# Performance work log

Hardware: AMD Instinct MI355X
Metric: run time of the kernel (lower is better)

The kernel has to match this reference:

```python
import jax, jax.numpy as jnp
import numpy as np

B = 128
C_IN = 1
HID = 256
LAT = 256
NC = 4096
NA = 16
G = 4
DH = 256        # DynamicsModel default hidden_dim
CE = DH // 2    # code/action embed dim
IMG = 64
COMMIT = 0.25
DN = ('NCHW', 'OIHW', 'NCHW')


def conv_s2(x, w, b):
    y = jax.lax.conv_general_dilated(x, w, (2, 2), ((1, 1), (1, 1)), dimension_numbers=DN)
    return y + b[None, :, None, None]


def deconv_s2(x, w, b):
    # torch ConvTranspose2d(k=4, s=2, p=1): flip kernel, swap I/O channels,
    wt = jnp.flip(w, (2, 3)).transpose(1, 0, 2, 3)
    y = jax.lax.conv_general_dilated(x, wt, (1, 1), ((2, 2), (2, 2)),
                                     lhs_dilation=(2, 2), dimension_numbers=DN)
    return y + b[None, :, None, None]


def setup_inputs():
    key = jax.random.key(0)
    ks = iter(jax.random.split(key, 64))

    def W(shape, fan_in):
        return jax.random.normal(next(ks), shape, jnp.float32) * np.float32(1.0 / np.sqrt(fan_in))

    inp = {}
    inp['x'] = jax.random.uniform(next(ks), (B, C_IN, IMG, IMG), jnp.float32)
    inp['x_next'] = jax.random.uniform(next(ks), (B, C_IN, IMG, IMG), jnp.float32)
    inp['action'] = jax.random.randint(next(ks), (B,), 0, NA)
    # encoder Conv2d weights: [out, in, 4, 4]
    inp['enc_w1'] = W((HID, C_IN, 4, 4), C_IN * 16); inp['enc_b1'] = jnp.zeros((HID,), jnp.float32)
    inp['enc_w2'] = W((HID, HID, 4, 4), HID * 16);   inp['enc_b2'] = jnp.zeros((HID,), jnp.float32)
    inp['enc_w3'] = W((HID, HID, 4, 4), HID * 16);   inp['enc_b3'] = jnp.zeros((HID,), jnp.float32)
    inp['enc_w4'] = W((LAT, HID, 4, 4), HID * 16);   inp['enc_b4'] = jnp.zeros((LAT,), jnp.float32)
    # decoder ConvTranspose2d weights: [in, out, 4, 4]
    inp['dec_w1'] = W((LAT, HID, 4, 4), LAT * 4);    inp['dec_b1'] = jnp.zeros((HID,), jnp.float32)
    inp['dec_w2'] = W((HID, HID, 4, 4), HID * 4);    inp['dec_b2'] = jnp.zeros((HID,), jnp.float32)
    inp['dec_w3'] = W((HID, HID, 4, 4), HID * 4);    inp['dec_b3'] = jnp.zeros((HID,), jnp.float32)
    inp['dec_w4'] = W((HID, C_IN, 4, 4), HID * 4);   inp['dec_b4'] = jnp.zeros((C_IN,), jnp.float32)
    inp['codebook'] = jax.random.normal(next(ks), (NC, LAT), jnp.float32)
    inp['code_embed'] = W((NC, CE), CE)
    inp['action_embed'] = W((NA, CE), CE)
    d_in = G * G * CE + CE
    inp['dyn_w1'] = W((d_in, DH), d_in);      inp['dyn_b1'] = jnp.zeros((DH,), jnp.float32)
    inp['dyn_w2'] = W((DH, DH), DH);          inp['dyn_b2'] = jnp.zeros((DH,), jnp.float32)
    inp['dyn_w3'] = W((DH, G * G * NC), DH);  inp['dyn_b3'] = jnp.zeros((G * G * NC,), jnp.float32)
    return inp


def reference(x, x_next, action,
              enc_w1, enc_b1, enc_w2, enc_b2, enc_w3, enc_b3, enc_w4, enc_b4,
              dec_w1, dec_b1, dec_w2, dec_b2, dec_w3, dec_b3, dec_w4, dec_b4,
              codebook, code_embed, action_embed,
              dyn_w1, dyn_b1, dyn_w2, dyn_b2, dyn_w3, dyn_b3):
    relu = jax.nn.relu
    sg = jax.lax.stop_gradient

    cb_sq = jnp.sum(codebook * codebook, axis=1)  # [NC]

    def encode(xi):
        h = relu(conv_s2(xi, enc_w1, enc_b1))
        h = relu(conv_s2(h, enc_w2, enc_b2))
        h = relu(conv_s2(h, enc_w3, enc_b3))
        z = conv_s2(h, enc_w4, enc_b4)                   # [B, LAT, G, G]
        zf = z.transpose(0, 2, 3, 1).reshape(-1, LAT)    # [B*G*G, LAT]
        # squared euclidean distances (argmin identical to cdist argmin)
        d2 = jnp.sum(zf * zf, axis=1, keepdims=True) - 2.0 * (zf @ codebook.T) + cb_sq
        codes = jnp.argmin(d2, axis=-1)                  # [B*G*G]
        zq = codebook[codes]                             # [B*G*G, LAT]
        return zf, zq, codes

    zf, zq, codes_flat = encode(x)
    commitment_loss = jnp.mean((zf - sg(zq)) ** 2)
    codebook_loss = jnp.mean((sg(zf) - zq) ** 2)
    vq_loss = codebook_loss + COMMIT * commitment_loss
    zq_st = zf + sg(zq - zf)                             # straight-through

    zq_grid = zq_st.reshape(-1, G, G, LAT).transpose(0, 3, 1, 2)  # [B, LAT, G, G]
    codes = codes_flat.reshape(-1, G, G)

    # decoder
    h = relu(deconv_s2(zq_grid, dec_w1, dec_b1))
    h = relu(deconv_s2(h, dec_w2, dec_b2))
    h = relu(deconv_s2(h, dec_w3, dec_b3))
    recon = jax.nn.sigmoid(deconv_s2(h, dec_w4, dec_b4))  # [B, 1, 64, 64]

    # dynamics
    ce = code_embed[codes].reshape(codes.shape[0], -1)    # [B, G*G*CE]
    ae = action_embed[action]                             # [B, CE]
    h2 = jnp.concatenate([ce, ae], axis=-1)
    h2 = relu(h2 @ dyn_w1 + dyn_b1)
    h2 = relu(h2 @ dyn_w2 + dyn_b2)
    next_logits = (h2 @ dyn_w3 + dyn_b3).reshape(-1, G, G, NC)

    # next-code target (no grad in original)
    _, _, nc_flat = encode(sg(x_next))
    next_codes_target = nc_flat.reshape(-1, G, G)

    return (recon, codes, commitment_loss, codebook_loss, vq_loss,
            next_logits, next_codes_target)
```

## Files before the change

kernel.cpp:

```cpp
#include <hip/hip_runtime.h>
#include <hip/hip_bf16.h>

typedef _Float16 f16;
typedef f16   f16x8 __attribute__((ext_vector_type(8)));
typedef short s16x8 __attribute__((ext_vector_type(8)));
typedef float f32x4 __attribute__((ext_vector_type(4)));
typedef unsigned short u16;

__device__ __forceinline__ f32x4 mfma_f16(f16x8 a, f16x8 b, f32x4 c){
  return __builtin_amdgcn_mfma_f32_16x16x32_f16(a,b,c,0,0,0);
}
__device__ __forceinline__ f32x4 mfma_bf16(s16x8 a, s16x8 b, f32x4 c){
  return __builtin_amdgcn_mfma_f32_16x16x32_bf16(a,b,c,0,0,0);
}
__device__ __forceinline__ u16 f2bf(float v){
  unsigned u = __float_as_uint(v);
  unsigned r = u + 0x7fffu + ((u>>16)&1u);
  return (u16)(r>>16);
}
__device__ __forceinline__ float bf2f(u16 v){ return __uint_as_float(((unsigned)v)<<16); }

#define N_B 128

#define OUT_RECON 0
#define OUT_CODES 524288
#define OUT_LC    526336
#define OUT_NL    526339
#define OUT_NCT   8914947

#define B_E1H  0ull
#define B_E1L  67108864ull
#define B_ZF   67108864ull
#define B_ZQ4  69206016ull
#define B_ZSQ  70254592ull
#define B_ACC  70287360ull
#define B_CODES 70320128ull
#define B_H1   70385664ull
#define B_H2   70516736ull
#define B_H2B  70647808ull
#define B_E3H  71303168ull
#define B_E3L  75497472ull
#define B_D1   71303168ull
#define B_D2   75497472ull
#define B_EMB  92274688ull
#define B_ZFH  100663296ull
#define B_ZFL  101711872ull
#define B_E2H  134217728ull
#define B_E2L  150994944ull
#define B_DOTS 134217728ull
#define B_WE2H 167772160ull
#define B_WE2L 169869312ull
#define B_WE3H 171966464ull
#define B_WE3L 174063616ull
#define B_WE4H 176160768ull
#define B_WE4L 178257920ull
#define B_WD1  180355072ull
#define B_WD2  182452224ull
#define B_WD3  184549376ull
#define B_CBSQ 186646528ull
#define B_ZERO 186712064ull
#define B_CBH  186712576ull
#define B_CBL  188809728ull

__global__ __launch_bounds__(256) void k_pack_enc(const float* __restrict__ w,
                                                  f16* __restrict__ Wh, f16* __restrict__ Wl){
  int o = blockIdx.x*256 + threadIdx.x;
  int j=o&7, l=(o>>3)&63, n=(o>>9)&15, icc=(o>>13)&7, tap=o>>16;
  int ic = icc*32 + (l>>4)*8 + j, oc = n*16 + (l&15);
  float v = w[((size_t)oc*256+ic)*16 + tap];
  f16 h = (f16)v;
  Wh[o]=h; Wl[o]=(f16)(v-(float)h);
}
__global__ __launch_bounds__(256) void k_pack_dec(const float* __restrict__ w, u16* __restrict__ Wp){
  int o = blockIdx.x*256 + threadIdx.x;
  int j=o&7, l=(o>>3)&63, n=(o>>9)&15, icc=(o>>13)&7, tap=o>>16;
  int ic = icc*32 + (l>>4)*8 + j, oc = n*16 + (l&15);
  Wp[o] = f2bf(w[((size_t)ic*256+oc)*16 + tap]);
}
__global__ __launch_bounds__(256) void k_pack_cb(const float* __restrict__ cb,
                                                 f16* __restrict__ H, f16* __restrict__ L){
  int s = blockIdx.x*256 + threadIdx.x;
  int n = s>>8, k = s&255;
  float v = cb[s];
  int nt = n>>4, lr2 = n&15, icc = k>>5, rr = k&31, lq2 = rr>>3, j = rr&7;
  size_t o = ((size_t)(nt*8+icc)*64 + lq2*16 + lr2)*8 + j;
  f16 h = (f16)v; H[o]=h; L[o]=(f16)(v-(float)h);
}
__global__ __launch_bounds__(256) void k_cbsq(const float* __restrict__ cb, float* __restrict__ cbsq,
                                              float* __restrict__ zg){
  int c = blockIdx.x*256 + threadIdx.x;
  if(blockIdx.x==0 && threadIdx.x<128) zg[threadIdx.x]=0.f;
  const float4* r4 = (const float4*)(cb + (size_t)c*256);
  float s = 0.f;
  for(int k=0;k<64;k++){ float4 v=r4[k]; s += v.x*v.x+v.y*v.y+v.z*v.z+v.w*v.w; }
  cbsq[c] = s;
}

__global__ __launch_bounds__(256) void k_conv1(const float* __restrict__ x, const float* __restrict__ w1,
                                               const float* __restrict__ b1,
                                               f16* __restrict__ Oh, f16* __restrict__ Ol){
  int b = blockIdx.x >> 5, oy = blockIdx.x & 31;
  int oc = threadIdx.x;
  __shared__ float xs[4][68];
  for(int i=threadIdx.x;i<264;i+=256){
    int rr=i/66, cc=i-rr*66;
    int iy=2*oy-1+rr, ix=cc-1;
    float v=0.f;
    if((unsigned)iy<64u && (unsigned)ix<64u) v = x[((size_t)b*64+iy)*64+ix];
    xs[rr][cc]=v;
  }
  __syncthreads();
  float wv[16];
  #pragma unroll
  for(int k=0;k<16;k++) wv[k]=w1[oc*16+k];
  float bv=b1[oc];
  for(int ox=0;ox<32;ox++){
    float acc=bv;
    int c0=2*ox;
    #pragma unroll
    for(int kh=0;kh<4;kh++)
      #pragma unroll
      for(int kw=0;kw<4;kw++) acc += wv[kh*4+kw]*xs[kh][c0+kw];
    float v = fmaxf(acc,0.f);
    f16 h=(f16)v;
    size_t o = (((size_t)b*32+oy)*32+ox)*256+oc;
    Oh[o]=h; Ol[o]=(f16)(v-(float)h);
  }
}

template<int MT, int HIN>
__global__ __launch_bounds__(256,2) void k_conv_v3(
    const f16* __restrict__ Ah, const f16* __restrict__ Al,
    const f16* __restrict__ Wh, const f16* __restrict__ Wl,
    const float* __restrict__ bias, f16* __restrict__ Oh, f16* __restrict__ Ol){
  constexpr int HOUT = HIN/2, HH = HOUT*HOUT;
  constexpr int ROWS = MT*16;
  constexpr int OYS  = ROWS/HOUT;
  static_assert(OYS*HOUT == ROWS, "block must cover whole oy rows");
  constexpr int IYT = 2*OYS + 2;
  constexpr int IXT = HIN + 2;
  constexpr int XS  = 40;
  constexpr int RS  = IXT*XS;
  constexpr int BUF = IYT*RS;
  constexpr int ITEMS = IYT*IXT*8;
  __shared__ f16 As[2*BUF];
  const int tid = threadIdx.x, lane = tid&63, w = tid>>6;
  const int lr = lane&15, lq = lane>>4;
  const int m_base = blockIdx.x*ROWS;
  const int b = m_base/HH;
  const int oy0 = (m_base - b*HH)/HOUT;
  const int iy0 = 2*oy0 - 1;
  const size_t gimg = (size_t)b*HIN*HIN*256;

  int rb[MT];
  #pragma unroll
  for(int t=0;t<MT;t++){
    int r = t*16 + lr;
    int oyl = r/HOUT, oxl = r - oyl*HOUT;
    rb[t] = (2*oyl)*RS + (2*oxl)*XS + lq*8;
  }

  f32x4 acc[MT][4];
  #pragma unroll
  for(int t=0;t<MT;t++)
    #pragma unroll
    for(int u=0;u<4;u++) acc[t][u] = (f32x4){0.f,0.f,0.f,0.f};

  for(int icc=0;icc<8;icc++){
    __syncthreads();
    for(int s=tid;s<ITEMS;s+=256){
      int c = s&7, posi = s>>3;
      int hl = c>>2, ck = c&3;
      int iyl = posi/IXT, ixl = posi - iyl*IXT;
      int iy = iy0 + iyl, ix = ixl - 1;
      f16x8 v = {0,0,0,0,0,0,0,0};
      if((unsigned)iy<(unsigned)HIN && (unsigned)ix<(unsigned)HIN){
        const f16* src = (hl ? Al : Ah) + gimg + (size_t)(iy*HIN+ix)*256 + icc*32 + ck*8;
        v = *(const f16x8*)src;
      }
      *(f16x8*)&As[hl*BUF + iyl*RS + ixl*XS + ck*8] = v;
    }
    __syncthreads();
    #pragma unroll
    for(int th=0;th<4;th++){
      #pragma unroll
      for(int tw=0;tw<4;tw++){
        const int tap = th*4 + tw;
        f16x8 a_h[MT], a_l[MT];
        #pragma unroll
        for(int t=0;t<MT;t++){
          int off = rb[t] + th*RS + tw*XS;
          a_h[t] = *(const f16x8*)&As[off];
          a_l[t] = *(const f16x8*)&As[BUF + off];
        }
        size_t wb = ((size_t)(tap*8+icc)*16 + w*4)*512 + lane*8;
        #pragma unroll
        for(int u=0;u<4;u++){
          f16x8 b_h = *(const f16x8*)(Wh + wb + u*512);
          f16x8 b_l = *(const f16x8*)(Wl + wb + u*512);
          #pragma unroll
          for(int t=0;t<MT;t++){
            acc[t][u] = mfma_f16(a_h[t], b_h, acc[t][u]);
            acc[t][u] = mfma_f16(a_h[t], b_l, acc[t][u]);
            acc[t][u] = mfma_f16(a_l[t], b_h, acc[t][u]);
          }
        }
      }
    }
  }
  #pragma unroll
  for(int t=0;t<MT;t++){
    #pragma unroll
    for(int u=0;u<4;u++){
      int n = (w*4+u)*16 + lr;
      float bv = bias[n];
      #pragma unroll
      for(int r=0;r<4;r++){
        int m = m_base + t*16 + lq*4 + r;
        float v = fmaxf(acc[t][u][r] + bv, 0.f);
        size_t o = (size_t)m*256 + n;
        f16 h=(f16)v; Oh[o]=h; Ol[o]=(f16)(v-(float)h);
      }
    }
  }
}

template<int MT>
__global__ __launch_bounds__(256) void k_conv4(
    const f16* __restrict__ Ah, const f16* __restrict__ Al,
    const f16* __restrict__ Wh, const f16* __restrict__ Wl,
    const float* __restrict__ bias, float* __restrict__ Of,
    f16* __restrict__ Zh, f16* __restrict__ Zl,
    const f16* __restrict__ Zp, int Hin){
  const int Hout = Hin>>1, HH = Hout*Hout;
  const int lane = threadIdx.x & 63, w = threadIdx.x >> 6;
  const int lr = lane & 15, lq = lane >> 4;
  const int m_base = blockIdx.x * (16*MT);
  int iyb[MT], ixb[MT], bb[MT];
  #pragma unroll
  for(int t=0;t<MT;t++){
    int m = m_base + t*16 + lr;
    int b = m/HH, rem = m - b*HH;
    int oy = rem/Hout, ox = rem - oy*Hout;
    bb[t]=b; iyb[t]=2*oy-1; ixb[t]=2*ox-1;
  }
  f32x4 acc[MT][4];
  #pragma unroll
  for(int t=0;t<MT;t++)
    #pragma unroll
    for(int u=0;u<4;u++) acc[t][u]=(f32x4){0.f,0.f,0.f,0.f};

  for(int tap=0;tap<16;tap++){
    int th=tap>>2, tw=tap&3;
    const f16* pH[MT]; const f16* pL[MT];
    #pragma unroll
    for(int t=0;t<MT;t++){
      int iy=iyb[t]+th, ix=ixb[t]+tw;
      bool val = ((unsigned)iy<(unsigned)Hin) && ((unsigned)ix<(unsigned)Hin);
      size_t o = (((size_t)bb[t]*Hin+iy)*Hin+ix)*256 + lq*8;
      pH[t] = val ? Ah+o : Zp;
      pL[t] = val ? Al+o : Zp;
    }
    #pragma unroll
    for(int icc=0;icc<8;icc++){
      f16x8 a_h[MT], a_l[MT];
      #pragma unroll
      for(int t=0;t<MT;t++){
        a_h[t] = *(const f16x8*)(pH[t] + icc*32);
        a_l[t] = *(const f16x8*)(pL[t] + icc*32);
      }
      size_t wb = ((size_t)(tap*8+icc)*16 + w*4)*512 + lane*8;
      #pragma unroll
      for(int u=0;u<4;u++){
        f16x8 b_h = *(const f16x8*)(Wh + wb + u*512);
        f16x8 b_l = *(const f16x8*)(Wl + wb + u*512);
        #pragma unroll
        for(int t=0;t<MT;t++){
          acc[t][u] = mfma_f16(a_h[t], b_h, acc[t][u]);
          acc[t][u] = mfma_f16(a_h[t], b_l, acc[t][u]);
          acc[t][u] = mfma_f16(a_l[t], b_h, acc[t][u]);
        }
      }
    }
  }
  #pragma unroll
  for(int t=0;t<MT;t++){
    #pragma unroll
    for(int u=0;u<4;u++){
      int n = (w*4+u)*16 + lr;
      float bv = bias[n];
      #pragma unroll
      for(int r=0;r<4;r++){
        int m = m_base + t*16 + lq*4 + r;
        float v = acc[t][u][r] + bv;
        size_t o = (size_t)m*256 + n;
        Of[o]=v;
        f16 h=(f16)v; Zh[o]=h; Zl[o]=(f16)(v-(float)h);
      }
    }
  }
}

template<int MT>
__global__ __launch_bounds__(256) void k_deconv_mfma(
    const u16* __restrict__ In, const u16* __restrict__ Wp,
    const float* __restrict__ bias, u16* __restrict__ Out,
    const u16* __restrict__ Zp, int H){
  const int Ho = H*2, HH = H*H;
  const int kh = blockIdx.y>>1, kw = blockIdx.y&1;
  const int lane = threadIdx.x & 63, w = threadIdx.x >> 6;
  const int lr = lane & 15, lq = lane >> 4;
  const int m_base = blockIdx.x * (16*MT);
  int jb[MT], ib[MT], bb[MT];
  #pragma unroll
  for(int t=0;t<MT;t++){
    int m = m_base + t*16 + lr;
    int b = m/HH, rem = m - b*HH;
    jb[t]=rem/H; ib[t]=rem-jb[t]*H; bb[t]=b;
  }
  f32x4 acc[MT][4];
  #pragma unroll
  for(int t=0;t<MT;t++)
    #pragma unroll
    for(int u=0;u<4;u++) acc[t][u]=(f32x4){0.f,0.f,0.f,0.f};

  #pragma unroll
  for(int dy=0;dy<2;dy++){
    #pragma unroll
    for(int dx=0;dx<2;dx++){
      int t16 = (kh+2*dy)*4 + (kw+2*dx);
      const u16* pA[MT];
      #pragma unroll
      for(int t=0;t<MT;t++){
        int r = jb[t]+(1-kh)-dy, c = ib[t]+(1-kw)-dx;
        bool val = ((unsigned)r<(unsigned)H) && ((unsigned)c<(unsigned)H);
        size_t o = (((size_t)bb[t]*H+r)*H+c)*256 + lq*8;
        pA[t] = val ? In+o : Zp;
      }
      #pragma unroll
      for(int icc=0;icc<8;icc++){
        s16x8 a[MT];
        #pragma unroll
        for(int t=0;t<MT;t++) a[t] = *(const s16x8*)(pA[t] + icc*32);
        size_t wb = ((size_t)(t16*8+icc)*16 + w*4)*512 + lane*8;
        #pragma unroll
        for(int u=0;u<4;u++){
          s16x8 bfr = *(const s16x8*)(Wp + wb + u*512);
          #pragma unroll
          for(int t=0;t<MT;t++) acc[t][u] = mfma_bf16(a[t], bfr, acc[t][u]);
        }
      }
    }
  }
  #pragma unroll
  for(int t=0;t<MT;t++){
    #pragma unroll
    for(int u=0;u<4;u++){
      int n = (w*4+u)*16 + lr;
      float bv = bias[n];
      #pragma unroll
      for(int r=0;r<4;r++){
        int m = m_base + t*16 + lq*4 + r;
        int b = m/HH, rem = m - b*HH;
        int j = rem/H, i = rem - j*H;
        int oy = 2*j + (1-kh), ox = 2*i + (1-kw);
        float v = fmaxf(acc[t][u][r] + bv, 0.f);
        Out[(((size_t)b*Ho+oy)*Ho+ox)*256 + n] = f2bf(v);
      }
    }
  }
}

__global__ __launch_bounds__(256) void k_dec4(const u16* __restrict__ In, const float* __restrict__ w4,
                                              const float* __restrict__ bias, float* __restrict__ out){
  __shared__ float wt[16][256];
  int t = threadIdx.x;
  for(int i=t;i<4096;i+=256) wt[i&15][i>>4] = w4[i];
  __syncthreads();
  int ox = t & 63, oy = (blockIdx.x<<2) + (t>>6), b = blockIdx.y;
  int iyh=(oy+1)>>1, kh=(oy+1)&1;
  int ixh=(ox+1)>>1, kw=(ox+1)&1;
  float acc = bias[0];
  #pragma unroll
  for(int dy=0;dy<2;dy++){
    int r = iyh-dy;
    if((unsigned)r>=32u) continue;
    #pragma unroll
    for(int dx=0;dx<2;dx++){
      int c = ixh-dx;
      if((unsigned)c>=32u) continue;
      const u16* p = In + (((size_t)b*32+r)*32+c)*256;
      int widx = (kh+2*dy)*4 + kw+2*dx;
      float s=0.f;
      for(int ic=0;ic<256;ic+=8){
        s16x8 vv = *(const s16x8*)(p+ic);
        const float* wr = &wt[widx][ic];
        #pragma unroll
        for(int q=0;q<8;q++) s += bf2f((u16)vv[q])*wr[q];
      }
      acc += s;
    }
  }
  out[(size_t)b*4096 + oy*64 + ox] = 1.f/(1.f+__expf(-acc));
}

__global__ __launch_bounds__(256) void k_zsq(const float* __restrict__ zf, float* __restrict__ zsq){
  int r=blockIdx.x, c=threadIdx.x;
  float v = zf[(size_t)r*256+c];
  __shared__ float red[256];
  red[c]=v*v; __syncthreads();
  for(int s=128;s>0;s>>=1){ if(c<s) red[c]+=red[c+s]; __syncthreads(); }
  if(c==0) zsq[r]=red[0];
}

__global__ __launch_bounds__(256,2) void k_dots(
    const f16* __restrict__ ZH, const f16* __restrict__ ZL,
    const f16* __restrict__ CH, const f16* __restrict__ CL, float* __restrict__ D){
  const int lane = threadIdx.x & 63, w = threadIdx.x >> 6;
  const int lr = lane & 15, lq = lane >> 4;
  const int m_base = blockIdx.y*64, nb = blockIdx.x;
  f32x4 acc[4][4];
  #pragma unroll
  for(int t=0;t<4;t++)
    #pragma unroll
    for(int u=0;u<4;u++) acc[t][u]=(f32x4){0.f,0.f,0.f,0.f};
  #pragma unroll
  for(int icc=0;icc<8;icc++){
    f16x8 ah[4], al[4];
    #pragma unroll
    for(int t=0;t<4;t++){
      size_t o = (size_t)(m_base + t*16 + lr)*256 + lq*8 + icc*32;
      ah[t] = *(const f16x8*)(ZH+o);
      al[t] = *(const f16x8*)(ZL+o);
    }
    #pragma unroll
    for(int u=0;u<4;u++){
      int nt = nb*16 + w*4 + u;
      size_t wb = ((size_t)(nt*8+icc)*64 + lane)*8;
      f16x8 b_h = *(const f16x8*)(CH+wb);
      f16x8 b_l = *(const f16x8*)(CL+wb);
      #pragma unroll
      for(int t=0;t<4;t++){
        acc[t][u] = mfma_f16(ah[t], b_h, acc[t][u]);
        acc[t][u] = mfma_f16(ah[t], b_l, acc[t][u]);
        acc[t][u] = mfma_f16(al[t], b_h, acc[t][u]);
      }
    }
  }
  #pragma unroll
  for(int t=0;t<4;t++)
    #pragma unroll
    for(int u=0;u<4;u++){
      int n = nb*256 + (w*4+u)*16 + lr;
      #pragma unroll
      for(int r=0;r<4;r++){
        int m = m_base + t*16 + lq*4 + r;
        D[(size_t)m*4096 + n] = acc[t][u][r];
      }
    }
}

__global__ __launch_bounds__(256) void k_argmin(const float* __restrict__ dots, const float* __restrict__ zsq,
                                                const float* __restrict__ cbsq, int* __restrict__ codes,
                                                float* __restrict__ out_codes){
  int r = blockIdx.x, t = threadIdx.x;
  float zs = zsq[r];
  float bv = 1e30f; int bi = 0x7fffffff;
  for(int c=t;c<4096;c+=256){
    float d = zs + cbsq[c] - 2.f*dots[(size_t)r*4096+c];
    if(d < bv || (d==bv && c<bi)){ bv=d; bi=c; }
  }
  __shared__ float sv[256]; __shared__ int si[256];
  sv[t]=bv; si[t]=bi; __syncthreads();
  for(int s=128;s>0;s>>=1){
    if(t<s){
      float v2=sv[t+s]; int i2=si[t+s];
      if(v2<sv[t] || (v2==sv[t] && i2<si[t])){ sv[t]=v2; si[t]=i2; }
    }
    __syncthreads();
  }
  if(t==0){ codes[r]=si[0]; out_codes[r]=(float)si[0]; }
}

__global__ void k_zero(float* a){ a[0]=0.f; }

__global__ __launch_bounds__(256) void k_zqloss(const float* __restrict__ zf, const float* __restrict__ cb,
                                                const int* __restrict__ codes, u16* __restrict__ zq4,
                                                float* __restrict__ accum){
  int r = blockIdx.x, c = threadIdx.x;
  int code = codes[r];
  float q = cb[(size_t)code*256 + c];
  float d = zf[(size_t)r*256+c] - q;
  zq4[(size_t)r*256 + c] = f2bf(q);
  __shared__ float red[256];
  red[c]=d*d; __syncthreads();
  for(int s=128;s>0;s>>=1){ if(c<s) red[c]+=red[c+s]; __syncthreads(); }
  if(c==0) atomicAdd(accum, red[0]);
}

__global__ void k_final(const float* __restrict__ accum, float* __restrict__ out){
  if(threadIdx.x==0){
    float L = accum[0]*(1.f/524288.f);
    out[0]=L; out[1]=L; out[2]=1.25f*L;
  }
}

__global__ __launch_bounds__(256) void k_embed(const int* __restrict__ codes, const int* __restrict__ action,
                                               const float* __restrict__ ce, const float* __restrict__ ae,
                                               float* __restrict__ emb){
  int b = blockIdx.x;
  for(int j=threadIdx.x;j<2176;j+=256){
    float v;
    if(j<2048){ int g=j>>7; v = ce[(size_t)codes[b*16+g]*128 + (j&127)]; }
    else      { v = ae[(size_t)action[b]*128 + (j-2048)]; }
    emb[(size_t)b*2176+j]=v;
  }
}

__global__ __launch_bounds__(256) void k_mlp(const float* __restrict__ in, const float* __restrict__ w,
                                             const float* __restrict__ bias, float* __restrict__ out,
                                             u16* __restrict__ outb, int K){
  int b = blockIdx.x, n = threadIdx.x;
  extern __shared__ float row[];
  for(int k=n;k<K;k+=256) row[k]=in[(size_t)b*K+k];
  __syncthreads();
  float acc = bias[n];
  for(int k=0;k<K;k++) acc += row[k]*w[(size_t)k*256+n];
  float v = fmaxf(acc,0.f);
  out[(size_t)b*256+n] = v;
  if(outb) outb[(size_t)b*256+n] = f2bf(v);
}

__global__ __launch_bounds__(256,2) void k_head(const u16* __restrict__ A,
                                                const float* __restrict__ w3,
                                                const float* __restrict__ b3,
                                                float* __restrict__ O){
  __shared__ u16 BS[8*64*8];
  const int tid = threadIdx.x, lane = tid&63, w = tid>>6;
  const int lr = lane&15, lq = lane>>4;
  const int nb = blockIdx.x;
  f32x4 acc[8][2];
  #pragma unroll
  for(int mt=0;mt<8;mt++)
    #pragma unroll
    for(int u=0;u<2;u++) acc[mt][u]=(f32x4){0.f,0.f,0.f,0.f};
  for(int icc=0;icc<8;icc++){
    __syncthreads();
    #pragma unroll
    for(int q=0;q<4;q++){
      int s = tid*16 + q*4;
      int kl = s>>7, nl = s&127;
      float4 v = *(const float4*)(w3 + (size_t)(icc*32+kl)*65536 + (size_t)nb*128 + nl);
      float vv[4] = {v.x,v.y,v.z,v.w};
      int j = kl&7, lqk = kl>>3;
      #pragma unroll
      for(int e=0;e<4;e++){
        int n2 = nl+e, ntl = n2>>4, lr2 = n2&15;
        BS[(ntl*64 + lqk*16 + lr2)*8 + j] = f2bf(vv[e]);
      }
    }
    __syncthreads();
    s16x8 a[8];
    #pragma unroll
    for(int mt=0;mt<8;mt++)
      a[mt] = *(const s16x8*)(A + (size_t)(mt*16+lr)*256 + icc*32 + lq*8);
    #pragma unroll
    for(int u=0;u<2;u++){
      int ntl = w*2+u;
      s16x8 bfr = *(const s16x8*)&BS[((size_t)ntl*64 + lane)*8];
      #pragma unroll
      for(int mt=0;mt<8;mt++) acc[mt][u] = mfma_bf16(a[mt], bfr, acc[mt][u]);
    }
  }
  #pragma unroll
  for(int mt=0;mt<8;mt++)
    #pragma unroll
    for(int u=0;u<2;u++){
      int n = nb*128 + (w*2+u)*16 + lr;
      float bv = b3[n];
      #pragma unroll
      for(int r=0;r<4;r++){
        int m = mt*16 + lq*4 + r;
        O[(size_t)m*65536 + n] = acc[mt][u][r] + bv;
      }
    }
}

extern "C" void kernel_launch(void* const* d_in, const int* in_sizes, int n_in,
                              void* d_out, int out_size, void* d_ws, size_t ws_size,
                              hipStream_t stream){
  (void)in_sizes; (void)n_in; (void)out_size; (void)ws_size;
  const float* x    = (const float*)d_in[0];
  const float* xn   = (const float*)d_in[1];
  const int*   act  = (const int*)  d_in[2];
  const float* ew1=(const float*)d_in[3];  const float* eb1=(const float*)d_in[4];
  const float* ew2=(const float*)d_in[5];  const float* eb2=(const float*)d_in[6];
  const float* ew3=(const float*)d_in[7];  const float* eb3=(const float*)d_in[8];
  const float* ew4=(const float*)d_in[9];  const float* eb4=(const float*)d_in[10];
  const float* dw1=(const float*)d_in[11]; const float* db1=(const float*)d_in[12];
  const float* dw2=(const float*)d_in[13]; const float* db2=(const float*)d_in[14];
  const float* dw3=(const float*)d_in[15]; const float* db3=(const float*)d_in[16];
  const float* dw4=(const float*)d_in[17]; const float* db4=(const float*)d_in[18];
  const float* cbk =(const float*)d_in[19];
  const float* cemb=(const float*)d_in[20];
  const float* aemb=(const float*)d_in[21];
  const float* yw1=(const float*)d_in[22]; const float* yb1=(const float*)d_in[23];
  const float* yw2=(const float*)d_in[24]; const float* yb2=(const float*)d_in[25];
  const float* yw3=(const float*)d_in[26]; const float* yb3=(const float*)d_in[27];
  float* out = (float*)d_out;

  char* wsb = (char*)d_ws;
  f16* E1H=(f16*)(wsb+B_E1H); f16* E1L=(f16*)(wsb+B_E1L);
  f16* E2H=(f16*)(wsb+B_E2H); f16* E2L=(f16*)(wsb+B_E2L);
  f16* E3H=(f16*)(wsb+B_E3H); f16* E3L=(f16*)(wsb+B_E3L);
  float* ZF=(float*)(wsb+B_ZF);
  f16* ZFH=(f16*)(wsb+B_ZFH); f16* ZFL=(f16*)(wsb+B_ZFL);
  u16* ZQ4=(u16*)(wsb+B_ZQ4);
  f16* WE2H=(f16*)(wsb+B_WE2H); f16* WE2L=(f16*)(wsb+B_WE2L);
  f16* WE3H=(f16*)(wsb+B_WE3H); f16* WE3L=(f16*)(wsb+B_WE3L);
  f16* WE4H=(f16*)(wsb+B_WE4H); f16* WE4L=(f16*)(wsb+B_WE4L);
  u16* WD1=(u16*)(wsb+B_WD1); u16* WD2=(u16*)(wsb+B_WD2); u16* WD3=(u16*)(wsb+B_WD3);
  f16* CBH=(f16*)(wsb+B_CBH); f16* CBL=(f16*)(wsb+B_CBL);
  float* ZSQ=(float*)(wsb+B_ZSQ); float* CBSQ=(float*)(wsb+B_CBSQ);
  float* EMB=(float*)(wsb+B_EMB); float* H1=(float*)(wsb+B_H1); float* H2=(float*)(wsb+B_H2);
  u16* H2B=(u16*)(wsb+B_H2B);
  float* ACC=(float*)(wsb+B_ACC); int* CODES=(int*)(wsb+B_CODES);
  float* ZG=(float*)(wsb+B_ZERO);
  const f16* Zf16=(const f16*)ZG; const u16* Zbf=(const u16*)ZG;
  float* DOTS=(float*)(wsb+B_DOTS);
  u16* D1=(u16*)(wsb+B_D1);
  u16* D2=(u16*)(wsb+B_D2);
  u16* D3=(u16*)(wsb+B_E1H);

  k_pack_enc<<<4096,256,0,stream>>>(ew2, WE2H, WE2L);
  k_pack_enc<<<4096,256,0,stream>>>(ew3, WE3H, WE3L);
  k_pack_enc<<<4096,256,0,stream>>>(ew4, WE4H, WE4L);
  k_pack_dec<<<4096,256,0,stream>>>(dw1, WD1);
  k_pack_dec<<<4096,256,0,stream>>>(dw2, WD2);
  k_pack_dec<<<4096,256,0,stream>>>(dw3, WD3);
  k_pack_cb <<<4096,256,0,stream>>>(cbk, CBH, CBL);
  k_cbsq<<<16,256,0,stream>>>(cbk, CBSQ, ZG);

  auto encode = [&](const float* img, float* code_out){
    k_conv1<<<4096,256,0,stream>>>(img, ew1, eb1, E1H, E1L);
    k_conv_v3<4,32><<<512,256,0,stream>>>(E1H,E1L, WE2H,WE2L, eb2, E2H,E2L);
    k_conv_v3<1,16><<<512,256,0,stream>>>(E2H,E2L, WE3H,WE3L, eb3, E3H,E3L);
    k_conv4<1><<<128,256,0,stream>>>(E3H,E3L, WE4H,WE4L, eb4, ZF, ZFH, ZFL, Zf16, 8);
    k_zsq<<<2048,256,0,stream>>>(ZF, ZSQ);
    k_dots<<<dim3(16,32),256,0,stream>>>(ZFH, ZFL, CBH, CBL, DOTS);
    k_argmin<<<2048,256,0,stream>>>(DOTS, ZSQ, CBSQ, CODES, code_out);
  };

  encode(x, out+OUT_CODES);
  k_zero<<<1,1,0,stream>>>(ACC);
  k_zqloss<<<2048,256,0,stream>>>(ZF, cbk, CODES, ZQ4, ACC);
  k_final<<<1,64,0,stream>>>(ACC, out+OUT_LC);

  k_deconv_mfma<1><<<dim3(128,4),256,0,stream>>>(ZQ4, WD1, db1, D1, Zbf, 4);
  k_deconv_mfma<4><<<dim3(128,4),256,0,stream>>>(D1,  WD2, db2, D2, Zbf, 8);
  k_deconv_mfma<4><<<dim3(512,4),256,0,stream>>>(D2,  WD3, db3, D3, Zbf, 16);
  k_dec4<<<dim3(16,N_B),256,0,stream>>>(D3, dw4, db4, out+OUT_RECON);

  k_embed<<<N_B,256,0,stream>>>(CODES, act, cemb, aemb, EMB);
  k_mlp<<<N_B,256,2176*4,stream>>>(EMB, yw1, yb1, H1, nullptr, 2176);
  k_mlp<<<N_B,256, 256*4,stream>>>(H1,  yw2, yb2, H2, H2B, 256);
  k_head<<<512,256,0,stream>>>(H2B, yw3, yb3, out+OUT_NL);

  encode(xn, out+OUT_NCT);
}
```

Measured before the change: 1.992 ms.

## Prefetch conv weights one tap ahead and precompute staging addresses

The encoder conv kernel now double-buffers the per-tap weight fragments in registers, loading the next tap's weights while the current tap's MFMAs run, so global weight load latency is hidden. The LDS staging loop's address arithmetic is hoisted out of the channel-chunk loop into per-thread precomputed offsets, and activation loads use nontemporal hints with 32-bit offsets. This adds register pressure from the doubled weight buffers, which may hurt occupancy under the 2-block launch bound. The 32-bit offsets and the Al-Ah pointer difference assume both buffers sit within one addressable range.

```diff
diff --git a/kernel.cpp b/kernel.cpp
--- a/kernel.cpp
+++ b/kernel.cpp
@@ -129,7 +129,7 @@
 }
 
 template<int MT, int HIN>
-__global__ __launch_bounds__(256,2) void k_conv_v3(
+__global__ __launch_bounds__(256,2) void k_conv_v4(
     const f16* __restrict__ Ah, const f16* __restrict__ Al,
     const f16* __restrict__ Wh, const f16* __restrict__ Wl,
     const float* __restrict__ bias, f16* __restrict__ Oh, f16* __restrict__ Ol){
@@ -143,6 +143,7 @@
   constexpr int RS  = IXT*XS;
   constexpr int BUF = IYT*RS;
   constexpr int ITEMS = IYT*IXT*8;
+  constexpr int NITEM = (ITEMS + 255)/256;
   __shared__ f16 As[2*BUF];
   const int tid = threadIdx.x, lane = tid&63, w = tid>>6;
   const int lr = lane&15, lq = lane>>4;
@@ -150,7 +151,22 @@
   const int b = m_base/HH;
   const int oy0 = (m_base - b*HH)/HOUT;
   const int iy0 = 2*oy0 - 1;
-  const size_t gimg = (size_t)b*HIN*HIN*256;
+  const int gb0 = b*HIN*HIN*256;
+  const int loff = (int)(Al - Ah);
+
+  int ls_it[NITEM], gb_it[NITEM];
+  #pragma unroll
+  for(int r=0;r<NITEM;r++){
+    int s = tid + r*256;
+    int c = s&7, posi = s>>3;
+    int hl = c>>2, ck = c&3;
+    int iyl = posi/IXT, ixl = posi - iyl*IXT;
+    int iy = iy0 + iyl, ix = ixl - 1;
+    int ls = hl*BUF + iyl*RS + ixl*XS + ck*8;
+    ls_it[r] = (s < ITEMS) ? ls : -1;
+    bool inb = ((unsigned)iy < (unsigned)HIN) && ((unsigned)ix < (unsigned)HIN);
+    gb_it[r] = inb ? (gb0 + (iy*HIN+ix)*256 + hl*loff + ck*8) : -1;
+  }
 
   int rb[MT];
   #pragma unroll
@@ -166,48 +182,50 @@
     #pragma unroll
     for(int u=0;u<4;u++) acc[t][u] = (f32x4){0.f,0.f,0.f,0.f};
 
+  f16x8 wbh[2][4], wbl[2][4];
+  #define LDW(TAP, BUFI) do{ \
+    size_t wb_ = ((size_t)((TAP)*8+icc)*16 + w*4)*512 + lane*8; \
+    _Pragma("unroll") \
+    for(int u_=0;u_<4;u_++){ \
+      wbh[BUFI][u_] = *(const f16x8*)(Wh + wb_ + u_*512); \
+      wbl[BUFI][u_] = *(const f16x8*)(Wl + wb_ + u_*512); \
+    } }while(0)
+
   for(int icc=0;icc<8;icc++){
+    LDW(0,0);
     __syncthreads();
-    for(int s=tid;s<ITEMS;s+=256){
-      int c = s&7, posi = s>>3;
-      int hl = c>>2, ck = c&3;
-      int iyl = posi/IXT, ixl = posi - iyl*IXT;
-      int iy = iy0 + iyl, ix = ixl - 1;
+    #pragma unroll
+    for(int r=0;r<NITEM;r++){
+      if(ls_it[r] < 0) continue;
       f16x8 v = {0,0,0,0,0,0,0,0};
-      if((unsigned)iy<(unsigned)HIN && (unsigned)ix<(unsigned)HIN){
-        const f16* src = (hl ? Al : Ah) + gimg + (size_t)(iy*HIN+ix)*256 + icc*32 + ck*8;
-        v = *(const f16x8*)src;
-      }
-      *(f16x8*)&As[hl*BUF + iyl*RS + ixl*XS + ck*8] = v;
+      int g = gb_it[r];
+      if(g >= 0) v = __builtin_nontemporal_load((const f16x8*)(Ah + (unsigned)g + icc*32));
+      *(f16x8*)&As[ls_it[r]] = v;
     }
     __syncthreads();
     #pragma unroll
-    for(int th=0;th<4;th++){
-      #pragma unroll
-      for(int tw=0;tw<4;tw++){
-        const int tap = th*4 + tw;
-        f16x8 a_h[MT], a_l[MT];
+    for(int tap=0;tap<16;tap++){
+      const int th = tap>>2, tw = tap&3, cur = tap&1;
+      if(tap<15){ const int nt_ = tap+1; LDW(nt_, cur^1); }
+      f16x8 a_h[MT], a_l[MT];
+      #pragma unroll
+      for(int t=0;t<MT;t++){
+        int off = rb[t] + th*RS + tw*XS;
+        a_h[t] = *(const f16x8*)&As[off];
+        a_l[t] = *(const f16x8*)&As[BUF + off];
+      }
+      #pragma unroll
+      for(int u=0;u<4;u++){
         #pragma unroll
         for(int t=0;t<MT;t++){
-          int off = rb[t] + th*RS + tw*XS;
-          a_h[t] = *(const f16x8*)&As[off];
-          a_l[t] = *(const f16x8*)&As[BUF + off];
+          acc[t][u] = mfma_f16(a_h[t], wbh[cur][u], acc[t][u]);
+          acc[t][u] = mfma_f16(a_h[t], wbl[cur][u], acc[t][u]);
+          acc[t][u] = mfma_f16(a_l[t], wbh[cur][u], acc[t][u]);
         }
-        size_t wb = ((size_t)(tap*8+icc)*16 + w*4)*512 + lane*8;
-        #pragma unroll
-        for(int u=0;u<4;u++){
-          f16x8 b_h = *(const f16x8*)(Wh + wb + u*512);
-          f16x8 b_l = *(const f16x8*)(Wl + wb + u*512);
-          #pragma unroll
-          for(int t=0;t<MT;t++){
-            acc[t][u] = mfma_f16(a_h[t], b_h, acc[t][u]);
-            acc[t][u] = mfma_f16(a_h[t], b_l, acc[t][u]);
-            acc[t][u] = mfma_f16(a_l[t], b_h, acc[t][u]);
-          }
-        }
-      }
-    }
-  }
+      }
+    }
+  }
+  #undef LDW
   #pragma unroll
   for(int t=0;t<MT;t++){
     #pragma unroll
@@ -643,8 +661,8 @@
 
   auto encode = [&](const float* img, float* code_out){
     k_conv1<<<4096,256,0,stream>>>(img, ew1, eb1, E1H, E1L);
-    k_conv_v3<4,32><<<512,256,0,stream>>>(E1H,E1L, WE2H,WE2L, eb2, E2H,E2L);
-    k_conv_v3<1,16><<<512,256,0,stream>>>(E2H,E2L, WE3H,WE3L, eb3, E3H,E3L);
+    k_conv_v4<4,32><<<512,256,0,stream>>>(E1H,E1L, WE2H,WE2L, eb2, E2H,E2L);
+    k_conv_v4<1,16><<<512,256,0,stream>>>(E2H,E2L, WE3H,WE3L, eb3, E3H,E3L);
     k_conv4<1><<<128,256,0,stream>>>(E3H,E3L, WE4H,WE4L, eb4, ZF, ZFH, ZFL, Zf16, 8);
     k_zsq<<<2048,256,0,stream>>>(ZF, ZSQ);
     k_dots<<<dim3(16,32),256,0,stream>>>(ZFH, ZFL, CBH, CBL, DOTS);
```

Result: slower. 2.122 ms (+6.6%).

## Add LDS-tiled implicit-GEMM conv kernel for encoder layer 2 and retune tiles

Applied to the files above, without the earlier changes.

Adds a new 512-thread conv kernel for the 32->16 encoder layer. It stages an input halo tile of hi/lo f16 activations in shared memory per 32-channel chunk and reuses it across all 16 taps. Each block covers 128 output rows with a 2x4 wave grid, which cuts redundant global loads of the im2col-style approach. The change also retunes the tile sizes for conv3 (MT 4, 128 blocks) and the third deconv (MT 8, 256 blocks), and adds an occupancy hint to the deconv kernel. These trade fewer, larger blocks and lower grid parallelism for more data reuse.

```diff
diff --git a/kernel.cpp b/kernel.cpp
--- a/kernel.cpp
+++ b/kernel.cpp
@@ -225,6 +225,99 @@
   }
 }
 
+__global__ __launch_bounds__(512,2) void k_conv_w(
+    const f16* __restrict__ Ah, const f16* __restrict__ Al,
+    const f16* __restrict__ Wh, const f16* __restrict__ Wl,
+    const float* __restrict__ bias, f16* __restrict__ Oh, f16* __restrict__ Ol){
+  constexpr int HIN = 32, HOUT = 16, HH = 256;
+  constexpr int ROWS = 128;
+  constexpr int IYT = 18, IXT = 34, XS = 40;
+  constexpr int RS  = IXT*XS;
+  constexpr int BUF = IYT*RS;
+  constexpr int ITEMS = IYT*IXT*8;
+  __shared__ f16 As[2*BUF];
+  const int tid = threadIdx.x, lane = tid&63, w = tid>>6;
+  const int lr = lane&15, lq = lane>>4;
+  const int wm = w>>2, wn = w&3;
+  const int m_base = blockIdx.x*ROWS;
+  const int b = m_base/HH;
+  const int oy0 = (m_base - b*HH)/HOUT;
+  const int iy0 = 2*oy0 - 1;
+  const size_t gimg = (size_t)b*HIN*HIN*256;
+
+  int rb[4];
+  #pragma unroll
+  for(int t=0;t<4;t++){
+    int r = wm*64 + t*16 + lr;
+    int oyl = r>>4, oxl = r&15;
+    rb[t] = (2*oyl)*RS + (2*oxl)*XS + lq*8;
+  }
+
+  f32x4 acc[4][4];
+  #pragma unroll
+  for(int t=0;t<4;t++)
+    #pragma unroll
+    for(int u=0;u<4;u++) acc[t][u] = (f32x4){0.f,0.f,0.f,0.f};
+
+  for(int icc=0;icc<8;icc++){
+    __syncthreads();
+    for(int s=tid;s<ITEMS;s+=512){
+      int c = s&7, posi = s>>3;
+      int hl = c>>2, ck = c&3;
+      int iyl = posi/IXT, ixl = posi - iyl*IXT;
+      int iy = iy0 + iyl, ix = ixl - 1;
+      f16x8 v = {0,0,0,0,0,0,0,0};
+      if((unsigned)iy<(unsigned)HIN && (unsigned)ix<(unsigned)HIN){
+        const f16* src = (hl ? Al : Ah) + gimg + (size_t)(iy*HIN+ix)*256 + icc*32 + ck*8;
+        v = *(const f16x8*)src;
+      }
+      *(f16x8*)&As[hl*BUF + iyl*RS + ixl*XS + ck*8] = v;
+    }
+    __syncthreads();
+    #pragma unroll
+    for(int th=0;th<4;th++){
+      #pragma unroll
+      for(int tw=0;tw<4;tw++){
+        const int tap = th*4 + tw;
+        f16x8 a_h[4], a_l[4];
+        #pragma unroll
+        for(int t=0;t<4;t++){
+          int off = rb[t] + th*RS + tw*XS;
+          a_h[t] = *(const f16x8*)&As[off];
+          a_l[t] = *(const f16x8*)&As[BUF + off];
+        }
+        size_t wb = ((size_t)(tap*8+icc)*16 + wn*4)*512 + lane*8;
+        #pragma unroll
+        for(int u=0;u<4;u++){
+          f16x8 b_h = *(const f16x8*)(Wh + wb + u*512);
+          f16x8 b_l = *(const f16x8*)(Wl + wb + u*512);
+          #pragma unroll
+          for(int t=0;t<4;t++){
+            acc[t][u] = mfma_f16(a_h[t], b_h, acc[t][u]);
+            acc[t][u] = mfma_f16(a_h[t], b_l, acc[t][u]);
+            acc[t][u] = mfma_f16(a_l[t], b_h, acc[t][u]);
+          }
+        }
+      }
+    }
+  }
+  #pragma unroll
+  for(int t=0;t<4;t++){
+    #pragma unroll
+    for(int u=0;u<4;u++){
+      int n = (wn*4+u)*16 + lr;
+      float bv = bias[n];
+      #pragma unroll
+      for(int r=0;r<4;r++){
+        int m = m_base + wm*64 + t*16 + lq*4 + r;
+        float v = fmaxf(acc[t][u][r] + bv, 0.f);
+        size_t o = (size_t)m*256 + n;
+        f16 h=(f16)v; Oh[o]=h; Ol[o]=(f16)(v-(float)h);
+      }
+    }
+  }
+}
+
 template<int MT>
 __global__ __launch_bounds__(256) void k_conv4(
     const f16* __restrict__ Ah, const f16* __restrict__ Al,
@@ -302,7 +395,7 @@
 }
 
 template<int MT>
-__global__ __launch_bounds__(256) void k_deconv_mfma(
+__global__ __launch_bounds__(256,2) void k_deconv_mfma(
     const u16* __restrict__ In, const u16* __restrict__ Wp,
     const float* __restrict__ bias, u16* __restrict__ Out,
     const u16* __restrict__ Zp, int H){
@@ -643,8 +736,8 @@
 
   auto encode = [&](const float* img, float* code_out){
     k_conv1<<<4096,256,0,stream>>>(img, ew1, eb1, E1H, E1L);
-    k_conv_v3<4,32><<<512,256,0,stream>>>(E1H,E1L, WE2H,WE2L, eb2, E2H,E2L);
-    k_conv_v3<1,16><<<512,256,0,stream>>>(E2H,E2L, WE3H,WE3L, eb3, E3H,E3L);
+    k_conv_w<<<256,512,0,stream>>>(E1H,E1L, WE2H,WE2L, eb2, E2H,E2L);
+    k_conv_v3<4,16><<<128,256,0,stream>>>(E2H,E2L, WE3H,WE3L, eb3, E3H,E3L);
     k_conv4<1><<<128,256,0,stream>>>(E3H,E3L, WE4H,WE4L, eb4, ZF, ZFH, ZFL, Zf16, 8);
     k_zsq<<<2048,256,0,stream>>>(ZF, ZSQ);
     k_dots<<<dim3(16,32),256,0,stream>>>(ZFH, ZFL, CBH, CBL, DOTS);
@@ -658,7 +751,7 @@
 
   k_deconv_mfma<1><<<dim3(128,4),256,0,stream>>>(ZQ4, WD1, db1, D1, Zbf, 4);
   k_deconv_mfma<4><<<dim3(128,4),256,0,stream>>>(D1,  WD2, db2, D2, Zbf, 8);
-  k_deconv_mfma<4><<<dim3(512,4),256,0,stream>>>(D2,  WD3, db3, D3, Zbf, 16);
+  k_deconv_mfma<8><<<dim3(256,4),256,0,stream>>>(D2,  WD3, db3, D3, Zbf, 16);
   k_dec4<<<dim3(16,N_B),256,0,stream>>>(D3, dw4, db4, out+OUT_RECON);
 
   k_embed<<<N_B,256,0,stream>>>(CODES, act, cemb, aemb, EMB);
```

After: 2.258 ms. 1.13x slower.
